# Kernel tuning notes

Measured on AMD Instinct MI355X. Metric: run time of the kernel, lower is better.

The kernel has to match this reference:

```python
import jax, jax.numpy as jnp
import numpy as np

# init_kwargs constants
MIN_T = 0.01
MAX_T = 0.5
TGT_MIN = 0.005
TGT_MAX = 0.03
W_MIN = 15.0
W_MAX = 5.0
W_CONT = 5.0
W_SIZE = 7.0
LESION_T = 0.3


def setup_inputs() -> dict:
    key = jax.random.key(0)
    pred = jax.random.uniform(key, (16, 1, 128, 128, 128), dtype=jnp.float32)
    return {"pred": pred}


def reference(pred):
    # pred: [B, 1, D, H, W]
    s = pred[:, 0]  # [B, D, H, W]
    B = s.shape[0]
    axes = (1, 2, 3)

    # -- min/max activation penalties (per-sample threshold means) --
    act = jnp.mean((s > MIN_T).astype(s.dtype), axis=axes)          # [B]
    loss = jax.nn.relu(TGT_MIN - act) * W_MIN
    high = jnp.mean((s > MAX_T).astype(s.dtype), axis=axes)
    loss = loss + jax.nn.relu(high - TGT_MAX) * W_MAX

    # -- continuity penalty: mean abs finite differences along D,H,W --
    d_grad = jnp.mean(jnp.abs(s[:, 1:] - s[:, :-1]), axis=axes)
    h_grad = jnp.mean(jnp.abs(s[:, :, 1:] - s[:, :, :-1]), axis=axes)
    w_grad = jnp.mean(jnp.abs(s[:, :, :, 1:] - s[:, :, :, :-1]), axis=axes)
    avg_grad = (d_grad + h_grad + w_grad) / 3.0
    has_lesion = jnp.any(s > LESION_T, axis=axes)
    loss = loss + jnp.where(has_lesion, jnp.minimum(avg_grad, 1.0), 0.0) * W_CONT

    # -- size-variance penalty over masked active values (unbiased std, torch.std) --
    mask = (s > MIN_T).astype(s.dtype)
    cnt = jnp.sum(mask, axis=axes)                                   # [B]
    cnt_safe = jnp.maximum(cnt, 1.0)
    m = jnp.sum(s * mask, axis=axes) / cnt_safe                      # masked mean [B]
    sq = jnp.sum(mask * (s - m[:, None, None, None]) ** 2, axis=axes)
    gate = (act > 0.001) & (cnt > 1.0)
    var = jnp.where(gate, sq / jnp.maximum(cnt - 1.0, 1.0), 1.0)     # guard sqrt/grad when gated off
    std = jnp.sqrt(var)
    rel_std = std / (m + 1e-6)
    pen = jnp.exp(-5.0 * rel_std)
    loss = loss + jnp.where(gate, pen, 0.0) * W_SIZE

    return jnp.sum(loss) / B
```

## Files before the change

kernel.cpp:

```cpp
#include <hip/hip_runtime.h>
#include <math.h>

#define MIN_T    0.01f
#define MAX_T    0.5f
#define LESION_T 0.3f

constexpr int NB       = 16;
constexpr int DIM      = 128;
constexpr int PLANE_F4 = DIM * DIM / 4;
constexpr int VOX      = DIM * DIM * DIM;
constexpr int THREADS  = 512;
constexpr int ROWS     = 16;
constexpr int HWBLKS   = DIM / ROWS;
constexpr int DSEGS    = 4;
constexpr int DPS      = DIM / DSEGS;
constexpr int NACC     = 8;
constexpr int SLOTS_PER_B = DSEGS * HWBLKS;
constexpr int NWAVES   = THREADS / 64;

__global__ __launch_bounds__(THREADS)
void partial_kernel(const float* __restrict__ pred, float* __restrict__ ws)
{
    const int seg   = blockIdx.x;
    const int hwblk = blockIdx.y;
    const int b     = blockIdx.z;
    const int tid   = (int)threadIdx.x;
    const int r     = tid >> 5;

    const int  h    = hwblk * ROWS + r;
    const bool do_h = (h < DIM - 1);
    const bool do_w = ((tid & 31) != 31);

    const float4* __restrict__ s4 =
        reinterpret_cast<const float4*>(pred + (size_t)b * VOX);

    const int d0    = seg * DPS;
    const int d_end = (seg == DSEGS - 1) ? (DIM - 1) : (d0 + DPS);

    float cnt_min = 0.f, cnt_max = 0.f, sum_d = 0.f, sum_h = 0.f,
          sum_w = 0.f, sm = 0.f, sm2 = 0.f, les = 0.f;
    const float4 zero4 = { 0.f, 0.f, 0.f, 0.f };

    auto process = [&](const float4& v, const float4& vh) {
        const float xs[4] = { v.x, v.y, v.z, v.w };
        #pragma unroll
        for (int j = 0; j < 4; ++j) {
            const float x  = xs[j];
            const float mk = (x > MIN_T) ? 1.0f : 0.0f;
            cnt_min += mk;
            cnt_max += (x > MAX_T)    ? 1.0f : 0.0f;
            les     += (x > LESION_T) ? 1.0f : 0.0f;
            sm      += x * mk;
            sm2     += x * x * mk;
        }
        sum_w += fabsf(v.y - v.x) + fabsf(v.z - v.y) + fabsf(v.w - v.z);
        const float nx = __shfl_down(v.x, 1, 64);
        if (do_w) sum_w += fabsf(nx - v.w);
        if (do_h) sum_h += fabsf(vh.x - v.x) + fabsf(vh.y - v.y)
                         + fabsf(vh.z - v.z) + fabsf(vh.w - v.w);
    };

    size_t base = (size_t)d0 * PLANE_F4 + hwblk * THREADS + tid;

    float4 v  = s4[base];
    float4 vh = do_h ? s4[base + 32] : zero4;

    for (int d = d0 + 1; d <= d_end; ++d) {
        base += PLANE_F4;
        const float4 nv  = s4[base];
        const float4 nvh = do_h ? s4[base + 32] : zero4;
        process(v, vh);
        sum_d += fabsf(nv.x - v.x) + fabsf(nv.y - v.y)
               + fabsf(nv.z - v.z) + fabsf(nv.w - v.w);
        v = nv; vh = nvh;
    }
    if (seg == DSEGS - 1)
        process(v, vh);

    float vals[NACC] = { cnt_min, cnt_max, sum_d, sum_h, sum_w, sm, sm2, les };
    #pragma unroll
    for (int vi = 0; vi < NACC; ++vi) {
        float x = vals[vi];
        #pragma unroll
        for (int off = 32; off > 0; off >>= 1)
            x += __shfl_down(x, off, 64);
        vals[vi] = x;
    }

    __shared__ float red[NWAVES][NACC];
    const int wave = tid >> 6;
    const int lane = tid & 63;
    if (lane == 0) {
        #pragma unroll
        for (int vi = 0; vi < NACC; ++vi) red[wave][vi] = vals[vi];
    }
    __syncthreads();
    if (tid < NACC) {
        float t = 0.f;
        #pragma unroll
        for (int w = 0; w < NWAVES; ++w) t += red[w][tid];
        const int slot = b * SLOTS_PER_B + hwblk * DSEGS + seg;
        ws[(size_t)slot * NACC + tid] = t;
    }
}

__global__ __launch_bounds__(512)
void finalize_kernel(const float* __restrict__ ws, float* __restrict__ out)
{
    const int tid = (int)threadIdx.x;
    const int b   = tid >> 5;
    const int k   = tid & 31;

    double a[NACC];
    const float* p = ws + ((size_t)(b * SLOTS_PER_B + k)) * NACC;
    #pragma unroll
    for (int vi = 0; vi < NACC; ++vi) a[vi] = (double)p[vi];

    #pragma unroll
    for (int vi = 0; vi < NACC; ++vi) {
        #pragma unroll
        for (int off = 16; off > 0; off >>= 1)
            a[vi] += __shfl_down(a[vi], off, 32);
    }

    __shared__ double bl[NB];
    if (k == 0) {
        const double cnt    = a[0];
        const double cntmax = a[1];
        const double sd     = a[2];
        const double sh     = a[3];
        const double sw     = a[4];
        const double sm     = a[5];
        const double sm2    = a[6];
        const double les    = a[7];

        const double inv_vox = 1.0 / (double)VOX;
        const double act  = cnt    * inv_vox;
        const double high = cntmax * inv_vox;

        double loss = fmax(0.005 - act, 0.0) * 15.0
                    + fmax(high - 0.03, 0.0) * 5.0;

        const double grad_den = 127.0 * 128.0 * 128.0;
        const double avg_grad = (sd + sh + sw) / (3.0 * grad_den);
        if (les > 0.5)
            loss += fmin(avg_grad, 1.0) * 5.0;

        const double cnt_safe = fmax(cnt, 1.0);
        const double m  = sm / cnt_safe;
        double sq = sm2 - 2.0 * m * sm + m * m * cnt;
        if (sq < 0.0) sq = 0.0;

        const bool gate = (act > 0.001) && (cnt > 1.0);
        if (gate) {
            const double var     = sq / fmax(cnt - 1.0, 1.0);
            const double rel_std = sqrt(var) / (m + 1e-6);
            loss += exp(-5.0 * rel_std) * 7.0;
        }
        bl[b] = loss;
    }
    __syncthreads();
    if (tid == 0) {
        double s = 0.0;
        #pragma unroll
        for (int i = 0; i < NB; ++i) s += bl[i];
        out[0] = (float)(s / (double)NB);
    }
}

extern "C" void kernel_launch(void* const* d_in, const int* in_sizes, int n_in,
                              void* d_out, int out_size, void* d_ws, size_t ws_size,
                              hipStream_t stream)
{
    const float* pred = (const float*)d_in[0];
    float* out        = (float*)d_out;
    float* ws         = (float*)d_ws;

    dim3 grid(DSEGS, HWBLKS, NB);
    partial_kernel<<<grid, THREADS, 0, stream>>>(pred, ws);
    finalize_kernel<<<1, 512, 0, stream>>>(ws, out);
}
```

Measured before the change: 192.0 us.

## Double depth segments and count thresholds with wave ballots instead of float adds

```diff
diff --git a/kernel.cpp b/kernel.cpp
--- a/kernel.cpp
+++ b/kernel.cpp
@@ -12,13 +12,13 @@
 constexpr int THREADS  = 512;
 constexpr int ROWS     = 16;
 constexpr int HWBLKS   = DIM / ROWS;
-constexpr int DSEGS    = 4;
+constexpr int DSEGS    = 8;
 constexpr int DPS      = DIM / DSEGS;
 constexpr int NACC     = 8;
 constexpr int SLOTS_PER_B = DSEGS * HWBLKS;
 constexpr int NWAVES   = THREADS / 64;
 
-__global__ __launch_bounds__(THREADS)
+__global__ __launch_bounds__(THREADS, 8)
 void partial_kernel(const float* __restrict__ pred, float* __restrict__ ws)
 {
     const int seg   = blockIdx.x;
@@ -37,21 +37,21 @@
     const int d0    = seg * DPS;
     const int d_end = (seg == DSEGS - 1) ? (DIM - 1) : (d0 + DPS);
 
-    float cnt_min = 0.f, cnt_max = 0.f, sum_d = 0.f, sum_h = 0.f,
-          sum_w = 0.f, sm = 0.f, sm2 = 0.f, les = 0.f;
+    unsigned int wmin = 0, wmax = 0, wles = 0;
+    float sum_d = 0.f, sum_h = 0.f, sum_w = 0.f, sm = 0.f, sm2 = 0.f;
     const float4 zero4 = { 0.f, 0.f, 0.f, 0.f };
 
     auto process = [&](const float4& v, const float4& vh) {
         const float xs[4] = { v.x, v.y, v.z, v.w };
         #pragma unroll
         for (int j = 0; j < 4; ++j) {
-            const float x  = xs[j];
-            const float mk = (x > MIN_T) ? 1.0f : 0.0f;
-            cnt_min += mk;
-            cnt_max += (x > MAX_T)    ? 1.0f : 0.0f;
-            les     += (x > LESION_T) ? 1.0f : 0.0f;
-            sm      += x * mk;
-            sm2     += x * x * mk;
+            const float x = xs[j];
+            wmin += (unsigned)__popcll(__ballot(x > MIN_T));
+            wmax += (unsigned)__popcll(__ballot(x > MAX_T));
+            wles += (unsigned)__popcll(__ballot(x > LESION_T));
+            const float y = (x > MIN_T) ? x : 0.0f;
+            sm  += y;
+            sm2  = fmaf(x, y, sm2);
         }
         sum_w += fabsf(v.y - v.x) + fabsf(v.z - v.y) + fabsf(v.w - v.z);
         const float nx = __shfl_down(v.x, 1, 64);
@@ -77,22 +77,28 @@
     if (seg == DSEGS - 1)
         process(v, vh);
 
-    float vals[NACC] = { cnt_min, cnt_max, sum_d, sum_h, sum_w, sm, sm2, les };
+    float fvals[5] = { sum_d, sum_h, sum_w, sm, sm2 };
     #pragma unroll
-    for (int vi = 0; vi < NACC; ++vi) {
-        float x = vals[vi];
+    for (int vi = 0; vi < 5; ++vi) {
+        float x = fvals[vi];
         #pragma unroll
         for (int off = 32; off > 0; off >>= 1)
             x += __shfl_down(x, off, 64);
-        vals[vi] = x;
+        fvals[vi] = x;
     }
 
     __shared__ float red[NWAVES][NACC];
     const int wave = tid >> 6;
     const int lane = tid & 63;
     if (lane == 0) {
-        #pragma unroll
-        for (int vi = 0; vi < NACC; ++vi) red[wave][vi] = vals[vi];
+        red[wave][0] = (float)wmin;
+        red[wave][1] = (float)wmax;
+        red[wave][2] = fvals[0];
+        red[wave][3] = fvals[1];
+        red[wave][4] = fvals[2];
+        red[wave][5] = fvals[3];
+        red[wave][6] = fvals[4];
+        red[wave][7] = (float)wles;
     }
     __syncthreads();
     if (tid < NACC) {
@@ -104,12 +110,12 @@
     }
 }
 
-__global__ __launch_bounds__(512)
+__global__ __launch_bounds__(1024)
 void finalize_kernel(const float* __restrict__ ws, float* __restrict__ out)
 {
     const int tid = (int)threadIdx.x;
-    const int b   = tid >> 5;
-    const int k   = tid & 31;
+    const int b   = tid >> 6;
+    const int k   = tid & 63;
 
     double a[NACC];
     const float* p = ws + ((size_t)(b * SLOTS_PER_B + k)) * NACC;
@@ -119,8 +125,8 @@
     #pragma unroll
     for (int vi = 0; vi < NACC; ++vi) {
         #pragma unroll
-        for (int off = 16; off > 0; off >>= 1)
-            a[vi] += __shfl_down(a[vi], off, 32);
+        for (int off = 32; off > 0; off >>= 1)
+            a[vi] += __shfl_down(a[vi], off, 64);
     }
 
     __shared__ double bl[NB];
@@ -178,5 +184,5 @@
 
     dim3 grid(DSEGS, HWBLKS, NB);
     partial_kernel<<<grid, THREADS, 0, stream>>>(pred, ws);
-    finalize_kernel<<<1, 512, 0, stream>>>(ws, out);
+    finalize_kernel<<<1, 1024, 0, stream>>>(ws, out);
 }
```

After: 194.1 us. No clear change (+1.1%).
